# Performance work log

Measured on AMD Instinct MI355X. Metric: run time of the kernel, lower is better.

The kernel has to match this reference:

```python
import jax, jax.numpy as jnp
import numpy as np

N_HEADS = 16
HEAD_DIM = 128  # d_model // n_heads


def rope(x):
    # x: [B, H, T, D]. Matches the torch module: interleaved even/odd split,
    # then concat([x1*cos - x2*sin, x1*sin + x2*cos], axis=-1).
    T, D = x.shape[2], x.shape[3]
    inv_freq = 1.0 / (10000.0 ** (jnp.arange(0, D, 2, dtype=x.dtype) / D))  # [D/2]
    freqs = jnp.arange(T, dtype=x.dtype)[:, None] * inv_freq[None, :]       # [T, D/2]
    sin, cos = jnp.sin(freqs), jnp.cos(freqs)                               # [T, D/2]
    x1, x2 = x[..., ::2], x[..., 1::2]                                      # [B,H,T,D/2]
    return jnp.concatenate([x1 * cos - x2 * sin, x1 * sin + x2 * cos], axis=-1)


def setup_inputs() -> dict:
    key = jax.random.key(0)
    ks = jax.random.split(key, 5)
    B, T, C = 2, 2048, 2048
    scale = 1.0 / np.sqrt(C)
    return {
        "x": jax.random.normal(ks[0], (B, T, C), dtype=jnp.float32),
        "W_qkv": jax.random.normal(ks[1], (3 * C, C), dtype=jnp.float32) * scale,
        "b_qkv": jnp.zeros((3 * C,), dtype=jnp.float32),
        "W_out": jax.random.normal(ks[2], (C, C), dtype=jnp.float32) * scale,
        "b_out": jnp.zeros((C,), dtype=jnp.float32),
    }


def reference(x, W_qkv, b_qkv, W_out, b_out):
    B, T, C = x.shape
    H, D = N_HEADS, HEAD_DIM
    qkv = x @ W_qkv.T + b_qkv                      # [B, T, 3C]
    qkv = qkv.reshape(B, T, 3, H, D)
    q, k, v = qkv[:, :, 0], qkv[:, :, 1], qkv[:, :, 2]  # [B, T, H, D]
    q = rope(jnp.transpose(q, (0, 2, 1, 3)))       # [B, H, T, D]
    k = rope(jnp.transpose(k, (0, 2, 1, 3)))
    v = jnp.transpose(v, (0, 2, 1, 3))
    scores = jnp.einsum("bhqd,bhkd->bhqk", q, k) / jnp.sqrt(jnp.asarray(D, x.dtype))
    causal = jnp.tril(jnp.ones((T, T), dtype=bool))
    scores = jnp.where(causal, scores, jnp.finfo(x.dtype).min)
    attn = jax.nn.softmax(scores, axis=-1)
    out = jnp.einsum("bhqk,bhkd->bhqd", attn, v)   # [B, H, T, D]
    out = jnp.transpose(out, (0, 2, 1, 3)).reshape(B, T, C)
    return out @ W_out.T + b_out
```

## Files before the change

kernel.cpp:

```cpp
#include <hip/hip_runtime.h>
#include <hip/hip_bf16.h>

typedef __attribute__((ext_vector_type(8))) short bf16x8;
typedef __attribute__((ext_vector_type(4))) float f32x4;

#define GLOAD_LDS16(gptr, lptr) \
  __builtin_amdgcn_global_load_lds((const __attribute__((address_space(1))) void*)(gptr), \
                                   (__attribute__((address_space(3))) void*)(lptr), 16, 0, 0)

__device__ __forceinline__ unsigned short f2b(float f) {
  union { float f; unsigned u; } x; x.f = f;
  unsigned r = x.u + 0x7fffu + ((x.u >> 16) & 1u);
  return (unsigned short)(r >> 16);
}
__device__ __forceinline__ float b2f(unsigned short u) {
  union { unsigned u; float f; } x; x.u = ((unsigned)u) << 16;
  return x.f;
}
__device__ __forceinline__ unsigned cvt_pk_bf16(float lo, float hi) {
  unsigned d;
  asm("v_cvt_pk_bf16_f32 %0, %1, %2" : "=v"(d) : "v"(lo), "v"(hi));
  return d;
}

__global__ void cast3_kernel(const float* __restrict__ x,
                             const float* __restrict__ wq,
                             const float* __restrict__ wo,
                             unsigned short* __restrict__ out)
{
  const long n1 = 8388608L;
  const long n2 = 20971520L;
  const long i = ((long)blockIdx.x * 256 + threadIdx.x) * 4;
  const float* src; long off;
  if (i < n1)      { src = x;  off = i; }
  else if (i < n2) { src = wq; off = i - n1; }
  else             { src = wo; off = i - n2; }
  const float4 v = *(const float4*)(src + off);
  ushort4 r;
  r.x = f2b(v.x); r.y = f2b(v.y); r.z = f2b(v.z); r.w = f2b(v.w);
  *(ushort4*)(out + i) = r;
}

template<int OUTF32>
__global__ __launch_bounds__(512, 4)
void gemm128(const unsigned short* __restrict__ A,
             const unsigned short* __restrict__ Bm,
             const float* __restrict__ bias,
             void* __restrict__ Cp,
             int M, int N, int K)
{
  __shared__ __align__(16) char Lds[73728];
  const int t  = threadIdx.x;
  const int l  = t & 63;
  const int w  = t >> 6;
  const int lr = l & 15;
  const int lkb = (l >> 4) << 4;
  const int wr = w >> 2;
  const int wc = w & 3;

  const int nwg = gridDim.x;
  const int wg  = (blockIdx.x & 7) * (nwg >> 3) + (blockIdx.x >> 3);
  const int NBN = N >> 8;
  const int bm = wg / NBN, bn = wg % NBN;

  const long K2 = (long)K * 2;
  const char* Ab = (const char*)A  + (long)(bm * 128) * K2;
  const char* Bb = (const char*)Bm + (long)(bn * 256) * K2;

  auto swz = [](int a) -> int { return a ^ (((a >> 7) & 3) << 4); };

  const int t16 = t << 4;
  const int da  = swz(t16);
  const long sa = (long)(da >> 6) * K2 + (da & 63);
  const int db0 = swz(t16), db1 = swz(8192 + t16);
  const long sb0 = (long)(db0 >> 6) * K2 + (db0 & 63);
  const long sb1 = (long)(db1 >> 6) * K2 + (db1 & 63);

  auto stage = [&](int g) {
    char* S = Lds + (g % 3) * 24576;
    const char* As = Ab + (long)g * 64;
    const char* Bs = Bb + (long)g * 64;
    GLOAD_LDS16(As + sa,  S + t16);
    GLOAD_LDS16(Bs + sb0, S + 8192 + t16);
    GLOAD_LDS16(Bs + sb1, S + 16384 + t16);
  };

  int aoff[4], boff[4];
#pragma unroll
  for (int mi = 0; mi < 4; ++mi) {
    const int a = ((wr * 64 + mi * 16 + lr) << 6) | lkb;
    aoff[mi] = swz(a);
  }
#pragma unroll
  for (int ni = 0; ni < 4; ++ni) {
    const int a = ((wc * 64 + ni * 16 + lr) << 6) | lkb;
    boff[ni] = 8192 + swz(a);
  }

  f32x4 acc[4][4] = {};
  const int NT = K >> 5;
  bf16x8 af[4], bfr[4];

  stage(0); stage(1);
  asm volatile("s_waitcnt vmcnt(3)" ::: "memory");
  __builtin_amdgcn_s_barrier();
  __builtin_amdgcn_sched_barrier(0);
#pragma unroll
  for (int mi = 0; mi < 4; ++mi) af[mi]  = *(const bf16x8*)(Lds + aoff[mi]);
#pragma unroll
  for (int ni = 0; ni < 4; ++ni) bfr[ni] = *(const bf16x8*)(Lds + boff[ni]);

  for (int tt = 0; tt < NT; ++tt) {
    if (tt + 2 < NT) stage(tt + 2);
    __builtin_amdgcn_s_setprio(1);
#pragma unroll
    for (int mi = 0; mi < 4; ++mi)
#pragma unroll
      for (int ni = 0; ni < 4; ++ni)
        acc[mi][ni] = __builtin_amdgcn_mfma_f32_16x16x32_bf16(af[mi], bfr[ni], acc[mi][ni], 0, 0, 0);
    __builtin_amdgcn_s_setprio(0);
    if (tt + 1 < NT) {
      if (tt + 2 < NT) asm volatile("s_waitcnt vmcnt(3)" ::: "memory");
      else             asm volatile("s_waitcnt vmcnt(0)" ::: "memory");
      __builtin_amdgcn_s_barrier();
      __builtin_amdgcn_sched_barrier(0);
      const char* S = Lds + ((tt + 1) % 3) * 24576;
#pragma unroll
      for (int mi = 0; mi < 4; ++mi) af[mi]  = *(const bf16x8*)(S + aoff[mi]);
#pragma unroll
      for (int ni = 0; ni < 4; ++ni) bfr[ni] = *(const bf16x8*)(S + boff[ni]);
    }
  }

  const int roff = (l >> 4) << 2;
  const int row0 = bm * 128 + wr * 64 + roff;
  const int col0 = bn * 256 + wc * 64 + lr;
  float bv[4];
#pragma unroll
  for (int ni = 0; ni < 4; ++ni) bv[ni] = bias ? bias[col0 + ni * 16] : 0.0f;
#pragma unroll
  for (int mi = 0; mi < 4; ++mi) {
#pragma unroll
    for (int r = 0; r < 4; ++r) {
      const long rb = (long)(row0 + mi * 16 + r) * N;
#pragma unroll
      for (int ni = 0; ni < 4; ++ni) {
        const float v = acc[mi][ni][r] + bv[ni];
        if (OUTF32) ((float*)Cp)[rb + col0 + ni * 16] = v;
        else ((unsigned short*)Cp)[rb + col0 + ni * 16] = f2b(v);
      }
    }
  }
}

__global__ void prep_kernel(const unsigned short* __restrict__ qkv,
                            unsigned short* __restrict__ Qr,
                            unsigned short* __restrict__ Kr,
                            unsigned short* __restrict__ Vt)
{
  const int T = 2048;
  const float C1 = 0.08838834764831845f * 1.4426950408889634f;
  __shared__ unsigned short ld[128][65];
  const int bh = blockIdx.y, tb = blockIdx.x;
  const int b = bh >> 4, h = bh & 15;
  const int t = threadIdx.x;

#pragma unroll
  for (int i = 0; i < 16; ++i) {
    const int idx = i * 256 + t;
    const int d  = idx & 63;
    const int tt = tb * 64 + (idx >> 6);
    const long base = ((long)(b * T + tt) * 3) * 2048 + h * 128;
    const float inv = exp2f(-(float)d * 0.2076205059304602f);
    const float fr = (float)tt * inv;
    float sn, cs;
    sincosf(fr, &sn, &cs);
    const float q1 = b2f(qkv[base + 2 * d]);
    const float q2 = b2f(qkv[base + 2 * d + 1]);
    const float k1 = b2f(qkv[base + 2048 + 2 * d]);
    const float k2 = b2f(qkv[base + 2048 + 2 * d + 1]);
    const long ob = ((long)bh * T + tt) * 128;
    Qr[ob + d]      = f2b(q1 * cs - q2 * sn);
    Qr[ob + 64 + d] = f2b(q1 * sn + q2 * cs);
    Kr[ob + d]      = f2b((k1 * cs - k2 * sn) * C1);
    Kr[ob + 64 + d] = f2b((k1 * sn + k2 * cs) * C1);
  }

#pragma unroll
  for (int i = 0; i < 32; ++i) {
    const int idx = i * 256 + t;
    const int d = idx & 127, tr = idx >> 7;
    ld[d][tr] = qkv[((long)(b * T + tb * 64 + tr) * 3 + 2) * 2048 + h * 128 + d];
  }
  __syncthreads();
#pragma unroll
  for (int i = 0; i < 32; ++i) {
    const int idx = i * 256 + t;
    const int tc = idx & 63, dr = idx >> 6;
    Vt[((long)bh * 128 + dr) * T + tb * 64 + tc] = ld[dr][tc];
  }
}

__global__ __launch_bounds__(256)
void attn_fwd(const unsigned short* __restrict__ Q,
              const unsigned short* __restrict__ Kg,
              const unsigned short* __restrict__ Vt,
              unsigned short* __restrict__ O, int T)
{
  __shared__ __align__(16) unsigned short Ks[2][64 * 128];
  __shared__ __align__(16) unsigned short Vs[128 * 64];
  const int t = threadIdx.x;
  const int w = t >> 6, l = t & 63;
  const int lr = l & 15;
  const int g  = l >> 4;
  const int g16 = g << 4;
  const int sw = (lr & 7) << 4;
  const int bh = blockIdx.x;
  const int qt = (gridDim.y - 1) - blockIdx.y;
  const int q0 = qt * 64 + w * 16;
  const long hbase = (long)bh * T * 128;
  const long hbase2 = hbase * 2;
  const long T2 = (long)T * 2;
  const int roff = g << 2;

  bf16x8 qf[4];
  const unsigned short* Qrow = Q + hbase + (long)(q0 + lr) * 128;
#pragma unroll
  for (int ds = 0; ds < 4; ++ds) qf[ds] = *(const bf16x8*)&Qrow[ds * 32 + (g16 >> 1)];

  f32x4 o[8] = {};
  float m = -INFINITY, lsum = 0.f;

  auto stageK = [&](int kt, int buf) {
#pragma unroll
    for (int c = 0; c < 4; ++c) {
      const int o2 = t * 16 + c * 4096;
      const int krow = o2 >> 8, kcb = o2 & 255;
      GLOAD_LDS16((const char*)Kg + hbase2 + (long)kt * 16384 + krow * 256 + (kcb ^ ((krow & 7) << 4)),
                  (char*)Ks[buf] + o2);
    }
  };
  auto stageV = [&](int kt) {
#pragma unroll
    for (int c = 0; c < 4; ++c) {
      const int o2 = t * 16 + c * 4096;
      const int vrow = o2 >> 7, vcb = o2 & 127;
      GLOAD_LDS16((const char*)Vt + (long)(bh * 128 + vrow) * T2 + (long)kt * 128 + (vcb ^ ((vrow & 7) << 4)),
                  (char*)Vs + o2);
    }
  };

  const int ntile = qt + 1;
  stageK(0, 0);
  stageV(0);
  __syncthreads();

  for (int kt = 0; kt < ntile; ++kt) {
    const int cur = kt & 1;
    if (kt + 1 < ntile) stageK(kt + 1, cur ^ 1);

    const char* KsB = (const char*)Ks[cur];

    f32x4 s[4] = {};
    __builtin_amdgcn_s_setprio(1);
#pragma unroll
    for (int tj = 0; tj < 4; ++tj)
#pragma unroll
      for (int ds = 0; ds < 4; ++ds) {
        bf16x8 kf = *(const bf16x8*)(KsB + (tj * 16 + lr) * 256 + ((ds * 64 + g16) ^ sw));
        s[tj] = __builtin_amdgcn_mfma_f32_16x16x32_bf16(kf, qf[ds], s[tj], 0, 0, 0);
      }
    __builtin_amdgcn_s_setprio(0);

    if (kt == qt) {
#pragma unroll
      for (int tj = 0; tj < 4; ++tj)
#pragma unroll
        for (int r = 0; r < 4; ++r)
          if (kt * 64 + tj * 16 + 4 * g + r > q0 + lr) s[tj][r] = -INFINITY;
    }

    float pmax = -INFINITY;
#pragma unroll
    for (int tj = 0; tj < 4; ++tj)
#pragma unroll
      for (int r = 0; r < 4; ++r) pmax = fmaxf(pmax, s[tj][r]);
    pmax = fmaxf(pmax, __shfl_xor(pmax, 16, 64));
    pmax = fmaxf(pmax, __shfl_xor(pmax, 32, 64));

    const bool need = !__all(pmax - m <= 8.0f);
    float corr = 1.0f;
    if (need) {
      const float mn = fmaxf(m, pmax);
      corr = exp2f(m - mn);
      m = mn;
    }

    float p[4][4];
    float rs = 0.f;
#pragma unroll
    for (int tj = 0; tj < 4; ++tj)
#pragma unroll
      for (int r = 0; r < 4; ++r) {
        const float pv = exp2f(s[tj][r] - m);
        p[tj][r] = pv;
        rs += pv;
      }
    rs += __shfl_xor(rs, 16, 64);
    rs += __shfl_xor(rs, 32, 64);
    lsum = lsum * corr + rs;

    unsigned D8[4][2];
#pragma unroll
    for (int tj = 0; tj < 4; ++tj) {
      D8[tj][0] = cvt_pk_bf16(p[tj][0], p[tj][1]);
      D8[tj][1] = cvt_pk_bf16(p[tj][2], p[tj][3]);
    }

    if (need) {
      float corrj[4];
#pragma unroll
      for (int j = 0; j < 4; ++j) corrj[j] = __shfl(corr, roff + j, 64);
#pragma unroll
      for (int nj = 0; nj < 8; ++nj)
#pragma unroll
        for (int j = 0; j < 4; ++j) o[nj][j] *= corrj[j];
    }

    if (kt + 1 < ntile) asm volatile("s_waitcnt vmcnt(4)" ::: "memory");
    else                asm volatile("s_waitcnt vmcnt(0)" ::: "memory");
    __builtin_amdgcn_s_barrier();
    __builtin_amdgcn_sched_barrier(0);

    __builtin_amdgcn_s_setprio(1);
#pragma unroll
    for (int ks = 0; ks < 2; ++ks) {
      union { unsigned u[4]; bf16x8 v; } pfu;
#pragma unroll
      for (int k2 = 0; k2 < 4; ++k2) {
        const int src = lr | ((2 * (g & 1) + (k2 >> 1)) << 4);
        const unsigned dwA = __shfl(D8[2 * ks][k2 & 1], src, 64);
        const unsigned dwB = __shfl(D8[2 * ks + 1][k2 & 1], src, 64);
        pfu.u[k2] = (g & 2) ? dwB : dwA;
      }
#pragma unroll
      for (int nj = 0; nj < 8; ++nj) {
        bf16x8 vf = *(const bf16x8*)((const char*)Vs + (nj * 16 + lr) * 128 + ((ks * 64 + g16) ^ sw));
        o[nj] = __builtin_amdgcn_mfma_f32_16x16x32_bf16(pfu.v, vf, o[nj], 0, 0, 0);
      }
    }
    __builtin_amdgcn_s_setprio(0);

    __syncthreads();
    if (kt + 1 < ntile) stageV(kt + 1);
  }

  const float inv = 1.0f / lsum;
  float invj[4];
#pragma unroll
  for (int j = 0; j < 4; ++j) invj[j] = __shfl(inv, roff + j, 64);
  const int b = bh >> 4, h = bh & 15;
#pragma unroll
  for (int nj = 0; nj < 8; ++nj)
#pragma unroll
    for (int j = 0; j < 4; ++j) {
      const int q = q0 + roff + j;
      const int d = nj * 16 + lr;
      O[(long)(b * T + q) * 2048 + h * 128 + d] = f2b(o[nj][j] * invj[j]);
    }
}

extern "C" void kernel_launch(void* const* d_in, const int* in_sizes, int n_in,
                              void* d_out, int out_size, void* d_ws, size_t ws_size,
                              hipStream_t stream)
{
  const int B = 2, T = 2048, C = 2048;
  const int M = B * T;
  const int N1 = 3 * C;
  const float* x    = (const float*)d_in[0];
  const float* Wqkv = (const float*)d_in[1];
  const float* bqkv = (const float*)d_in[2];
  const float* Wout = (const float*)d_in[3];
  const float* bout = (const float*)d_in[4];
  float* out = (float*)d_out;

  char* p = (char*)d_ws;
  unsigned short* xb    = (unsigned short*)p; p += (size_t)M * C * 2;
  unsigned short* wqkvb = (unsigned short*)p; p += (size_t)N1 * C * 2;
  unsigned short* woutb = (unsigned short*)p; p += (size_t)C * C * 2;
  unsigned short* qkv   = (unsigned short*)p; p += (size_t)M * N1 * 2;
  unsigned short* Qr    = (unsigned short*)p; p += (size_t)M * C * 2;
  unsigned short* Kr    = (unsigned short*)p; p += (size_t)M * C * 2;
  unsigned short* Vt    = (unsigned short*)p; p += (size_t)M * C * 2;
  unsigned short* Ob    = xb;

  const long ncast = (long)M * C + (long)N1 * C + (long)C * C;
  cast3_kernel<<<(int)(ncast / 1024), 256, 0, stream>>>(x, Wqkv, Wout, xb);

  gemm128<0><<<dim3((M / 128) * (N1 / 256)), 512, 0, stream>>>(xb, wqkvb, bqkv, qkv, M, N1, C);

  prep_kernel<<<dim3(T / 64, 32), 256, 0, stream>>>(qkv, Qr, Kr, Vt);

  attn_fwd<<<dim3(32, T / 64), 256, 0, stream>>>(Qr, Kr, Vt, Ob, T);

  gemm128<1><<<dim3((M / 128) * (C / 256)), 512, 0, stream>>>(Ob, woutb, bout, out, M, C, C);
}
```

Before: 285.4 us.

## Fuse RoPE and Q/K head-layout scatter into QKV GEMM epilogue

The QKV projection GEMM epilogue now applies RoPE directly, pairing even and odd columns with a lane shuffle. It writes rotated and pre-scaled Q/K in per-head layout plus V in per-head layout, so the intermediate qkv buffer is no longer materialised. The old prep kernel becomes a V-transpose-only kernel, which removes a full read of the qkv buffer and part of the prep work. In exchange the epilogue does extra sincos math and scattered 2-byte stores. It also uses the faster, less precise __sincosf with arguments up to 2047 radians, which may reduce accuracy.

```diff
diff --git a/kernel.cpp b/kernel.cpp
--- a/kernel.cpp
+++ b/kernel.cpp
@@ -41,12 +41,15 @@
   *(ushort4*)(out + i) = r;
 }
 
-template<int OUTF32>
+template<int MODE>
 __global__ __launch_bounds__(512, 4)
 void gemm128(const unsigned short* __restrict__ A,
              const unsigned short* __restrict__ Bm,
              const float* __restrict__ bias,
              void* __restrict__ Cp,
+             unsigned short* __restrict__ Qr,
+             unsigned short* __restrict__ Kr,
+             unsigned short* __restrict__ Vr,
              int M, int N, int K)
 {
   __shared__ __align__(16) char Lds[73728];
@@ -138,66 +141,77 @@
   float bv[4];
 #pragma unroll
   for (int ni = 0; ni < 4; ++ni) bv[ni] = bias ? bias[col0 + ni * 16] : 0.0f;
-#pragma unroll
-  for (int mi = 0; mi < 4; ++mi) {
-#pragma unroll
-    for (int r = 0; r < 4; ++r) {
-      const long rb = (long)(row0 + mi * 16 + r) * N;
-#pragma unroll
-      for (int ni = 0; ni < 4; ++ni) {
-        const float v = acc[mi][ni][r] + bv[ni];
-        if (OUTF32) ((float*)Cp)[rb + col0 + ni * 16] = v;
-        else ((unsigned short*)Cp)[rb + col0 + ni * 16] = f2b(v);
-      }
-    }
-  }
-}
-
-__global__ void prep_kernel(const unsigned short* __restrict__ qkv,
-                            unsigned short* __restrict__ Qr,
-                            unsigned short* __restrict__ Kr,
-                            unsigned short* __restrict__ Vt)
+
+  if (MODE == 1) {
+#pragma unroll
+    for (int mi = 0; mi < 4; ++mi) {
+#pragma unroll
+      for (int r = 0; r < 4; ++r) {
+        const long rb = (long)(row0 + mi * 16 + r) * N;
+#pragma unroll
+        for (int ni = 0; ni < 4; ++ni)
+          ((float*)Cp)[rb + col0 + ni * 16] = acc[mi][ni][r] + bv[ni];
+      }
+    }
+  } else {
+    const float C1 = 0.08838834764831845f * 1.4426950408889634f;
+    const int sec = col0 >> 11;
+    const int cq0 = col0 & 2047;
+    const int parity = col0 & 1;
+    int hh[4], dd[4], jj[4];
+    float invf[4];
+#pragma unroll
+    for (int ni = 0; ni < 4; ++ni) {
+      const int c = cq0 + ni * 16;
+      hh[ni] = c >> 7;
+      dd[ni] = c & 127;
+      jj[ni] = dd[ni] >> 1;
+      invf[ni] = exp2f(-(float)jj[ni] * 0.2076205059304602f);
+    }
+#pragma unroll
+    for (int mi = 0; mi < 4; ++mi) {
+#pragma unroll
+      for (int r = 0; r < 4; ++r) {
+        const int row = row0 + mi * 16 + r;
+        const int b = row >> 11, tt = row & 2047;
+#pragma unroll
+        for (int ni = 0; ni < 4; ++ni) {
+          const float val = acc[mi][ni][r] + bv[ni];
+          if (sec == 2) {
+            Vr[((long)((b << 4) | hh[ni]) * 2048 + tt) * 128 + dd[ni]] = f2b(val);
+          } else {
+            const float pv = __shfl_xor(val, 1, 64);
+            float sn, cs;
+            __sincosf((float)tt * invf[ni], &sn, &cs);
+            float out = parity ? fmaf(pv, sn, val * cs) : fmaf(val, cs, -(pv * sn));
+            const long addr = ((long)((b << 4) | hh[ni]) * 2048 + tt) * 128 + jj[ni] + (parity << 6);
+            if (sec == 0) Qr[addr] = f2b(out);
+            else          Kr[addr] = f2b(out * C1);
+          }
+        }
+      }
+    }
+  }
+}
+
+__global__ void vtrans_kernel(const unsigned short* __restrict__ Vr,
+                              unsigned short* __restrict__ Vt)
 {
-  const int T = 2048;
-  const float C1 = 0.08838834764831845f * 1.4426950408889634f;
   __shared__ unsigned short ld[128][65];
   const int bh = blockIdx.y, tb = blockIdx.x;
-  const int b = bh >> 4, h = bh & 15;
   const int t = threadIdx.x;
-
-#pragma unroll
-  for (int i = 0; i < 16; ++i) {
-    const int idx = i * 256 + t;
-    const int d  = idx & 63;
-    const int tt = tb * 64 + (idx >> 6);
-    const long base = ((long)(b * T + tt) * 3) * 2048 + h * 128;
-    const float inv = exp2f(-(float)d * 0.2076205059304602f);
-    const float fr = (float)tt * inv;
-    float sn, cs;
-    sincosf(fr, &sn, &cs);
-    const float q1 = b2f(qkv[base + 2 * d]);
-    const float q2 = b2f(qkv[base + 2 * d + 1]);
-    const float k1 = b2f(qkv[base + 2048 + 2 * d]);
-    const float k2 = b2f(qkv[base + 2048 + 2 * d + 1]);
-    const long ob = ((long)bh * T + tt) * 128;
-    Qr[ob + d]      = f2b(q1 * cs - q2 * sn);
-    Qr[ob + 64 + d] = f2b(q1 * sn + q2 * cs);
-    Kr[ob + d]      = f2b((k1 * cs - k2 * sn) * C1);
-    Kr[ob + 64 + d] = f2b((k1 * sn + k2 * cs) * C1);
-  }
-
 #pragma unroll
   for (int i = 0; i < 32; ++i) {
     const int idx = i * 256 + t;
     const int d = idx & 127, tr = idx >> 7;
-    ld[d][tr] = qkv[((long)(b * T + tb * 64 + tr) * 3 + 2) * 2048 + h * 128 + d];
+    ld[d][tr] = Vr[((long)bh * 2048 + tb * 64 + tr) * 128 + d];
   }
   __syncthreads();
 #pragma unroll
   for (int i = 0; i < 32; ++i) {
     const int idx = i * 256 + t;
     const int tc = idx & 63, dr = idx >> 6;
-    Vt[((long)bh * 128 + dr) * T + tb * 64 + tc] = ld[dr][tc];
+    Vt[((long)bh * 128 + dr) * 2048 + tb * 64 + tc] = ld[dr][tc];
   }
 }
 
@@ -388,7 +402,7 @@
   unsigned short* xb    = (unsigned short*)p; p += (size_t)M * C * 2;
   unsigned short* wqkvb = (unsigned short*)p; p += (size_t)N1 * C * 2;
   unsigned short* woutb = (unsigned short*)p; p += (size_t)C * C * 2;
-  unsigned short* qkv   = (unsigned short*)p; p += (size_t)M * N1 * 2;
+  unsigned short* Vr    = (unsigned short*)p; p += (size_t)M * C * 2;
   unsigned short* Qr    = (unsigned short*)p; p += (size_t)M * C * 2;
   unsigned short* Kr    = (unsigned short*)p; p += (size_t)M * C * 2;
   unsigned short* Vt    = (unsigned short*)p; p += (size_t)M * C * 2;
@@ -397,11 +411,13 @@
   const long ncast = (long)M * C + (long)N1 * C + (long)C * C;
   cast3_kernel<<<(int)(ncast / 1024), 256, 0, stream>>>(x, Wqkv, Wout, xb);
 
-  gemm128<0><<<dim3((M / 128) * (N1 / 256)), 512, 0, stream>>>(xb, wqkvb, bqkv, qkv, M, N1, C);
-
-  prep_kernel<<<dim3(T / 64, 32), 256, 0, stream>>>(qkv, Qr, Kr, Vt);
+  gemm128<2><<<dim3((M / 128) * (N1 / 256)), 512, 0, stream>>>(
+      xb, wqkvb, bqkv, nullptr, Qr, Kr, Vr, M, N1, C);
+
+  vtrans_kernel<<<dim3(T / 64, 32), 256, 0, stream>>>(Vr, Vt);
 
   attn_fwd<<<dim3(32, T / 64), 256, 0, stream>>>(Qr, Kr, Vt, Ob, T);
 
-  gemm128<1><<<dim3((M / 128) * (C / 256)), 512, 0, stream>>>(Ob, woutb, bout, out, M, C, C);
-}
+  gemm128<1><<<dim3((M / 128) * (C / 256)), 512, 0, stream>>>(
+      Ob, woutb, bout, out, nullptr, nullptr, nullptr, M, C, C);
+}
```

Measured after the change: 281.6 us. Within noise of the previous version (-1.3%).
